# Optimization experiments

Hardware: AMD Instinct MI355X
Metric: run time of the kernel (lower is better)

## Reference

```python
import jax, jax.numpy as jnp
import numpy as np

N, C, D, K = 4096, 512, 64, 10  # samples, clusters (c_max), feature_dim, num_classes
KAPPA_N = 10.0


def setup_inputs() -> dict:
    key = jax.random.key(0)
    k1, k2, k3, k4, k5, k6 = jax.random.split(key, 6)
    data = jax.random.normal(k1, (N, D), dtype=jnp.float32)
    labels = jax.random.randint(k2, (N,), 0, K)
    # cluster support counts n >= kappa_n (mature clusters)
    n = jax.random.uniform(k3, (C,), dtype=jnp.float32) * 90.0 + KAPPA_N
    mu = jax.random.normal(k4, (C, D), dtype=jnp.float32) * 2.0
    # S is the scatter matrix; covariance Sigma = S / n must be SPD, so
    # build S = n * (0.1 * A A^T + 0.5 I)
    A = jax.random.normal(k5, (C, D, D), dtype=jnp.float32)
    AAT = jnp.einsum('cij,ckj->cik', A, A) / D
    S = n[:, None, None] * (0.1 * AAT + 0.5 * jnp.eye(D, dtype=jnp.float32))
    # one-hot class label per cluster
    cls = jax.random.randint(k6, (C,), 0, K)
    cluster_labels = jax.nn.one_hot(cls, K, dtype=jnp.int32)
    return {"data": data, "labels": labels, "n": n, "mu": mu, "S": S,
            "cluster_labels": cluster_labels}


def reference(data, labels, n, mu, S, cluster_labels):
    # Inference path of eGAUSSp.forward: for each sample z,
    #   Gamma_j = exp(-0.5 * (z - mu_j)^T (S_j / n_j)^{-1} (z - mu_j))   (all c clusters)
    #   scores  = defuzzify = sum_j Gamma_j * onehot(label_j) / sum_j Gamma_j
    # Vectorized over the batch (no cross-sample dependence in eval mode).
    eps = jnp.asarray(1e-6, data.dtype)
    Sigma = S / n[:, None, None] + eps * jnp.eye(S.shape[-1], dtype=data.dtype)  # [C,D,D]
    Sinv = jnp.linalg.inv(Sigma)                                                  # [C,D,D]
    diff = data[:, None, :] - mu[None, :, :]          # [N,C,D]
    tmp = jnp.einsum('ncd,cde->nce', diff, Sinv)      # [N,C,D]
    d2 = jnp.einsum('nce,nce->nc', tmp, diff)         # [N,C] squared Mahalanobis
    Gamma = jnp.exp(-0.5 * d2)                        # [N,C] activations
    lab_f = cluster_labels.astype(data.dtype)         # [C,K]
    scores = (Gamma @ lab_f) / (jnp.sum(Gamma, axis=1, keepdims=True) + 1e-12)  # [N,K]
    pred = jnp.argmax(scores, axis=1)
    clusters = jnp.argmax(Gamma, axis=1)
    return scores, pred, clusters
```

## Files before the change

### kernel.cpp

```cpp
#include <hip/hip_runtime.h>
#include <hip/hip_bf16.h>
#include <math.h>

#define NS 4096
#define NC 512
#define ND 64
#define NK 10
#define NPAIR 2080
#define KP 2176
#define BOFF 2080
#define KOFF 2144
#define ZB 1024
#define QB 2048
#define KSPLIT 4
#define KT_PER 17

typedef __attribute__((ext_vector_type(8))) short short8;
typedef __attribute__((ext_vector_type(4))) float floatx4;

__device__ inline unsigned short f2b(float x) {
    __hip_bfloat16 h = __float2bfloat16(x);
    return __builtin_bit_cast(unsigned short, h);
}
__device__ inline float b2f(unsigned short u) {
    __hip_bfloat16 h = __builtin_bit_cast(__hip_bfloat16, u);
    return __bfloat162float(h);
}

__device__ inline float rlane(float v, int k) {
    return __builtin_bit_cast(float, __builtin_amdgcn_readlane(__builtin_bit_cast(int, v), k));
}

__device__ inline void gl16(const void* g, void* l) {
    __builtin_amdgcn_global_load_lds(
        (const __attribute__((address_space(1))) unsigned int*)g,
        (__attribute__((address_space(3))) unsigned int*)l, 16, 0, 0);
}

__device__ inline uchar2 ed_decode(int p) {
    if (p < NPAIR) {
        const float s = sqrtf((float)(16641 - 8 * p));
        int e = (int)((129.0f - s) * 0.5f);
        int off = e * 64 - (e * (e - 1)) / 2;
        const int offn = off + (64 - e);
        if (p >= offn) { off = offn; ++e; }
        else if (p < off) { off -= (65 - e); --e; }
        return make_uchar2((unsigned char)e, (unsigned char)(e + (p - off)));
    } else if (p < KOFF) return make_uchar2((unsigned char)(p - BOFF), 64);
    else if (p == KOFF)  return make_uchar2(64, 64);
    return make_uchar2(65, 65);
}

__global__ __launch_bounds__(256, 4) void prep_kernel(
    const float* __restrict__ data, const float* __restrict__ S,
    const float* __restrict__ n, const float* __restrict__ mu,
    const int* __restrict__ clab,
    unsigned short* __restrict__ Qh, unsigned short* __restrict__ Ql,
    unsigned short* __restrict__ Bph, unsigned short* __restrict__ Bpl,
    float* __restrict__ d2, float* __restrict__ labf)
{
    __shared__ float AcolS[ND * (ND + 1)];
    __shared__ float cbuf[ND];
    __shared__ float rowbuf[2][ND];
    __shared__ float kksS[1];
    __shared__ float zq[2][66];

    if (blockIdx.x >= NC + ZB) {
        const int qb = blockIdx.x - (NC + ZB);
        const int half = threadIdx.x >> 7;
        const int i = threadIdx.x & 127;
        const int row = qb * 2 + half;
        if (i < 64) zq[half][i] = data[(size_t)row * ND + i];
        else if (i == 64) { zq[half][64] = 1.0f; zq[half][65] = 0.0f; }
        __syncthreads();
        const float* __restrict__ zr = zq[half];
        unsigned short* __restrict__ qh = Qh + (size_t)row * KP;
        unsigned short* __restrict__ ql = Ql + (size_t)row * KP;
        #pragma unroll
        for (int t = 0; t < 4; ++t) {
            const int p0 = t * 512 + i * 4;
            uchar2 ed = ed_decode(p0);
            unsigned short h4[4], l4[4];
            #pragma unroll
            for (int r = 0; r < 4; ++r) {
                const float v = zr[ed.x] * zr[ed.y];
                h4[r] = f2b(v);
                l4[r] = f2b(v - b2f(h4[r]));
                ed = (ed.y < 63) ? make_uchar2(ed.x, (unsigned char)(ed.y + 1))
                                 : make_uchar2((unsigned char)(ed.x + 1),
                                               (unsigned char)(ed.x + 1));
            }
            *(short4*)&qh[p0] = make_short4((short)h4[0], (short)h4[1],
                                            (short)h4[2], (short)h4[3]);
            *(short4*)&ql[p0] = make_short4((short)l4[0], (short)l4[1],
                                            (short)l4[2], (short)l4[3]);
        }
        {
            const int p = 2048 + i;
            const uchar2 ed = ed_decode(p);
            const float v = zr[ed.x] * zr[ed.y];
            const unsigned short h = f2b(v);
            const unsigned short l = f2b(v - b2f(h));
            qh[p] = h;
            ql[p] = l;
        }
        return;
    }

    if (blockIdx.x >= NC) {
        const size_t base = (size_t)(blockIdx.x - NC) * 2048 + threadIdx.x * 8;
        *(float4*)&d2[base]     = make_float4(0.f, 0.f, 0.f, 0.f);
        *(float4*)&d2[base + 4] = make_float4(0.f, 0.f, 0.f, 0.f);
        return;
    }

    const int c = blockIdx.x;
    const int tid = threadIdx.x;
    const int j = tid & 63;
    const int w = tid >> 6;
    const int rbase = w * 16;

    const float inv_nc = 1.0f / n[c];
    const float* __restrict__ Sc = S + (size_t)c * ND * ND + j;

    float4 B0, B1, B2, B3;
#define LOADT(u) \
    const float t##u##0 = Sc[(rbase + 4*(u) + 0) * ND]; \
    const float t##u##1 = Sc[(rbase + 4*(u) + 1) * ND]; \
    const float t##u##2 = Sc[(rbase + 4*(u) + 2) * ND]; \
    const float t##u##3 = Sc[(rbase + 4*(u) + 3) * ND];
    LOADT(0) LOADT(1) LOADT(2) LOADT(3)
#undef LOADT
    __builtin_amdgcn_sched_barrier(0);
#define SCALE(u) { \
    const float x0 = t##u##0 * inv_nc; \
    const float x1 = t##u##1 * inv_nc; \
    const float x2 = t##u##2 * inv_nc; \
    const float x3 = t##u##3 * inv_nc; \
    B##u.x = (rbase + 4*(u) + 0 == j) ? x0 + 1e-6f : x0; \
    B##u.y = (rbase + 4*(u) + 1 == j) ? x1 + 1e-6f : x1; \
    B##u.z = (rbase + 4*(u) + 2 == j) ? x2 + 1e-6f : x2; \
    B##u.w = (rbase + 4*(u) + 3 == j) ? x3 + 1e-6f : x3; }
    SCALE(0) SCALE(1) SCALE(2) SCALE(3)
#undef SCALE

#define UPD4(u, K) {                                                  \
    const float c0 = rlane(B##u.x, K);                                \
    const float c1 = rlane(B##u.y, K);                                \
    const float c2 = rlane(B##u.z, K);                                \
    const float c3 = rlane(B##u.w, K);                                \
    B##u.x = (om && (4*(u)+0 == ((K)&15))) ? rowk : B##u.x * am - c0 * rowk; \
    B##u.y = (om && (4*(u)+1 == ((K)&15))) ? rowk : B##u.y * am - c1 * rowk; \
    B##u.z = (om && (4*(u)+2 == ((K)&15))) ? rowk : B##u.z * am - c2 * rowk; \
    B##u.w = (om && (4*(u)+3 == ((K)&15))) ? rowk : B##u.w * am - c3 * rowk; \
}
#define STEPC(TL, C, K) {                                             \
    if (w == ((K) >> 4)) {                                            \
        const float rp = B##TL.C;          \
        const float pv = rlane(rp, K);             \
        const float ip = 1.0f / pv;                                   \
        rowbuf[(K) & 1][j] = (j == (K)) ? ip : rp * ip;               \
    }                                                                 \
    __syncthreads();                                                  \
    const float rowk = rowbuf[(K) & 1][j];                            \
    const float am = (j == (K)) ? 0.0f : 1.0f;                        \
    const bool om = (w == ((K) >> 4));                                \
    UPD4(0, K) UPD4(1, K) UPD4(2, K) UPD4(3, K)                       \
}
#define STEP4(T, TL) STEPC(TL, x, 4*(T)+0) STEPC(TL, y, 4*(T)+1) \
                     STEPC(TL, z, 4*(T)+2) STEPC(TL, w, 4*(T)+3)
#define FOR16P(M) M(0,0) M(1,1) M(2,2) M(3,3) M(4,0) M(5,1) M(6,2) M(7,3) \
                  M(8,0) M(9,1) M(10,2) M(11,3) M(12,0) M(13,1) M(14,2) M(15,3)
    FOR16P(STEP4)
#undef FOR16P
#undef STEP4
#undef STEPC
#undef UPD4

#define MIR(u) *(float4*)&AcolS[j * (ND + 1) + rbase + 4*(u)] = B##u;
    MIR(0) MIR(1) MIR(2) MIR(3)
#undef MIR
    __syncthreads();

    if (w == 0) {
        const float* __restrict__ muc = mu + (size_t)c * ND;
        float y = 0.f;
        #pragma unroll
        for (int t = 0; t < 16; ++t) {
            const float4 v = *(const float4*)&AcolS[j * (ND + 1) + 4 * t];
            y += v.x * muc[4*t]     + v.y * muc[4*t + 1]
               + v.z * muc[4*t + 2] + v.w * muc[4*t + 3];
        }
        cbuf[j] = -2.0f * y;
        float kk = muc[j] * y;
        #pragma unroll
        for (int off = 32; off > 0; off >>= 1) kk += __shfl_down(kk, off);
        if (j == 0) {
            kksS[0] = kk;
            int lab = 0;
            for (int q = 0; q < NK; ++q) if (clab[c * NK + q] != 0) lab = q;
            labf[c] = (float)lab;
        }
    }
    __syncthreads();
    const float kks = kksS[0];

    unsigned short* __restrict__ ph = Bph + (size_t)c * KP;
    unsigned short* __restrict__ pl = Bpl + (size_t)c * KP;
    #pragma unroll
    for (int i = 0; i < 9; ++i) {
        const int t = w + 4 * i;
        if (t < KP / 64) {
            const int p = t * 64 + j;
            float val;
            if (p < NPAIR) {
                const uchar2 ed = ed_decode(p);
                val = (ed.x == ed.y) ? AcolS[ed.x * (ND + 1) + ed.x]
                    : (AcolS[ed.y * (ND + 1) + ed.x] + AcolS[ed.x * (ND + 1) + ed.y]);
            } else if (p < KOFF) val = cbuf[p - BOFF];
            else if (p == KOFF)  val = kks;
            else                 val = 0.f;
            const unsigned short h = f2b(val);
            const unsigned short l = f2b(val - b2f(h));
            ph[p] = h;
            pl[p] = l;
        }
    }
}

__global__ __launch_bounds__(256, 5) void gemm_kernel(
    const unsigned short* __restrict__ Qh, const unsigned short* __restrict__ Ql,
    const unsigned short* __restrict__ Bph, const unsigned short* __restrict__ Bpl,
    float* __restrict__ d2)
{
    __shared__ unsigned short AhS[2][64 * 32], AlS[2][64 * 32];
    __shared__ unsigned short BhS[2][64 * 32], BlS[2][64 * 32];

    const int tid  = threadIdx.x;
    const int lane = tid & 63, w = tid >> 6;
    const int quad = lane >> 4, rlo = lane & 15;

    const int m0 = blockIdx.x * 64;
    const int n0 = blockIdx.y * 64;
    const int koff0 = blockIdx.z * KT_PER * 32;

    const int srow = tid >> 2;
    const int sswz = (tid & 3) ^ ((srow >> 2) & 3);
    const unsigned short* aGh = Qh + (size_t)(m0 + srow) * KP + koff0 + sswz * 8;
    const unsigned short* aGl = Ql + (size_t)(m0 + srow) * KP + koff0 + sswz * 8;
    const unsigned short* bGh = Bph + (size_t)(n0 + srow) * KP + koff0 + sswz * 8;
    const unsigned short* bGl = Bpl + (size_t)(n0 + srow) * KP + koff0 + sswz * 8;
    const int swz8 = (quad ^ ((rlo >> 2) & 3)) * 8;

    floatx4 acc[4] = {};

#define STAGE(b, t) {                                                 \
        const int _ko = (t) * 32;                                     \
        gl16(aGh + _ko, &AhS[b][tid * 8]);                            \
        gl16(aGl + _ko, &AlS[b][tid * 8]);                            \
        gl16(bGh + _ko, &BhS[b][tid * 8]);                            \
        gl16(bGl + _ko, &BlS[b][tid * 8]);                            \
    }

    STAGE(0, 0)
    STAGE(1, 1)
    asm volatile("s_waitcnt vmcnt(4)" ::: "memory");
    __builtin_amdgcn_s_barrier();
    __builtin_amdgcn_sched_barrier(0);

    for (int kt = 0; kt < KT_PER; ++kt) {
        const int cur = kt & 1;

        short8 ah[4], al[4], bh, bl;
        #pragma unroll
        for (int i = 0; i < 4; ++i) {
            ah[i] = *(const short8*)&AhS[cur][(i * 16 + rlo) * 32 + swz8];
            al[i] = *(const short8*)&AlS[cur][(i * 16 + rlo) * 32 + swz8];
        }
        {
            const int r = w * 16 + rlo;
            bh = *(const short8*)&BhS[cur][r * 32 + swz8];
            bl = *(const short8*)&BlS[cur][r * 32 + swz8];
        }

        __builtin_amdgcn_s_setprio(1);
        #pragma unroll
        for (int i = 0; i < 4; ++i) {
            acc[i] = __builtin_amdgcn_mfma_f32_16x16x32_bf16(al[i], bh, acc[i], 0, 0, 0);
            acc[i] = __builtin_amdgcn_mfma_f32_16x16x32_bf16(ah[i], bl, acc[i], 0, 0, 0);
            acc[i] = __builtin_amdgcn_mfma_f32_16x16x32_bf16(ah[i], bh, acc[i], 0, 0, 0);
        }
        __builtin_amdgcn_s_setprio(0);

        asm volatile("s_waitcnt lgkmcnt(0)" ::: "memory");
        __builtin_amdgcn_s_barrier();

        if (kt < KT_PER - 2) STAGE(cur, kt + 2)

        if (kt < KT_PER - 2) {
            asm volatile("s_waitcnt vmcnt(4)" ::: "memory");
        } else {
            asm volatile("s_waitcnt vmcnt(0)" ::: "memory");
        }
        __builtin_amdgcn_s_barrier();
        __builtin_amdgcn_sched_barrier(0);
    }
#undef STAGE

    #pragma unroll
    for (int i = 0; i < 4; ++i) {
        const int m = m0 + i * 16 + quad * 4;
        const int nn = n0 + w * 16 + rlo;
        #pragma unroll
        for (int r = 0; r < 4; ++r)
            atomicAdd(&d2[(size_t)(m + r) * NC + nn], acc[i][r]);
    }
}

__global__ __launch_bounds__(256) void score_kernel(
    const float* __restrict__ d2, const float* __restrict__ labf,
    float* __restrict__ out)
{
    const int s = blockIdx.x * 4 + (threadIdx.x >> 6);
    const int l = threadIdx.x & 63;

    float numer[NK];
    #pragma unroll
    for (int q = 0; q < NK; ++q) numer[q] = 0.f;
    float denom = 0.f, gmax = -1.f;
    int gidx = 0;

    #pragma unroll
    for (int i = 0; i < NC / 256; ++i) {
        const int c0 = i * 256 + l * 4;
        const float4 v = *(const float4*)&d2[(size_t)s * NC + c0];
        #pragma unroll
        for (int r = 0; r < 4; ++r) {
            const int c = c0 + r;
            const float G = __expf(-0.5f * ((const float*)&v)[r]);
            denom += G;
            const int lab = (int)labf[c];
            #pragma unroll
            for (int q = 0; q < NK; ++q) numer[q] += (q == lab) ? G : 0.f;
            if (G > gmax) { gmax = G; gidx = c; }
        }
    }

    #pragma unroll
    for (int off = 32; off > 0; off >>= 1) {
        const float og = __shfl_down(gmax, off);
        const int   oi = __shfl_down(gidx, off);
        if (og > gmax || (og == gmax && oi < gidx)) { gmax = og; gidx = oi; }
        denom += __shfl_down(denom, off);
        #pragma unroll
        for (int q = 0; q < NK; ++q) numer[q] += __shfl_down(numer[q], off);
    }

    if (l == 0) {
        const float inv = 1.0f / (denom + 1e-12f);
        float best = -1.f; int pk = 0;
        #pragma unroll
        for (int q = 0; q < NK; ++q) {
            const float sc = numer[q] * inv;
            out[(size_t)s * NK + q] = sc;
            if (sc > best) { best = sc; pk = q; }
        }
        out[(size_t)NS * NK + s]      = (float)pk;
        out[(size_t)NS * NK + NS + s] = (float)gidx;
    }
}

extern "C" void kernel_launch(void* const* d_in, const int* in_sizes, int n_in,
                              void* d_out, int out_size, void* d_ws, size_t ws_size,
                              hipStream_t stream)
{
    const float* data = (const float*)d_in[0];
    const float* n    = (const float*)d_in[2];
    const float* mu   = (const float*)d_in[3];
    const float* S    = (const float*)d_in[4];
    const int*   clab = (const int*)d_in[5];

    char* w = (char*)d_ws;
    unsigned short* Qh  = (unsigned short*)(w);
    unsigned short* Ql  = (unsigned short*)(w + 17825792);
    unsigned short* Bph = (unsigned short*)(w + 35651584);
    unsigned short* Bpl = (unsigned short*)(w + 37879808);
    float* d2   = (float*)(w + 40108032);
    float* labf = (float*)(w + 48496640);

    hipLaunchKernelGGL(prep_kernel,  dim3(NC + ZB + QB), dim3(256), 0, stream,
                       data, S, n, mu, clab, Qh, Ql, Bph, Bpl, d2, labf);
    hipLaunchKernelGGL(gemm_kernel,  dim3(NS / 64, NC / 64, KSPLIT), dim3(256), 0, stream,
                       Qh, Ql, Bph, Bpl, d2);
    hipLaunchKernelGGL(score_kernel, dim3(NS / 4), dim3(256), 0, stream,
                       d2, labf, (float*)d_out);
}
```

Measured before the change: 150.6 us.

## Drop split-K atomics; use 64x32 GEMM tiles over full K with direct stores

Replaces the 4-way split-K GEMM, which needed a zeroing pass in the prep kernel and atomicAdd accumulation, with a non-split GEMM. Each block now computes a 64x32 tile over the full K=2176 and writes d2 with plain stores. The grid shrinks from 64x8x4 to 64x16 blocks, but each block runs a 68-step K loop. B tiles are halved, so each wave holds 2 accumulators instead of 4, and occupancy is raised to 6. This removes atomic traffic and the d2 memset, at the cost of less A reuse per block (A is loaded twice as often) and fewer blocks to hide latency.

```diff
diff --git a/kernel.cpp b/kernel.cpp
--- a/kernel.cpp
+++ b/kernel.cpp
@@ -10,10 +10,8 @@
 #define KP 2176
 #define BOFF 2080
 #define KOFF 2144
-#define ZB 1024
 #define QB 2048
-#define KSPLIT 4
-#define KT_PER 17
+#define KT 68
 
 typedef __attribute__((ext_vector_type(8))) short short8;
 typedef __attribute__((ext_vector_type(4))) float floatx4;
@@ -57,7 +55,7 @@
     const int* __restrict__ clab,
     unsigned short* __restrict__ Qh, unsigned short* __restrict__ Ql,
     unsigned short* __restrict__ Bph, unsigned short* __restrict__ Bpl,
-    float* __restrict__ d2, float* __restrict__ labf)
+    float* __restrict__ labf)
 {
     __shared__ float AcolS[ND * (ND + 1)];
     __shared__ float cbuf[ND];
@@ -65,8 +63,8 @@
     __shared__ float kksS[1];
     __shared__ float zq[2][66];
 
-    if (blockIdx.x >= NC + ZB) {
-        const int qb = blockIdx.x - (NC + ZB);
+    if (blockIdx.x >= NC) {
+        const int qb = blockIdx.x - NC;
         const int half = threadIdx.x >> 7;
         const int i = threadIdx.x & 127;
         const int row = qb * 2 + half;
@@ -104,13 +102,6 @@
             qh[p] = h;
             ql[p] = l;
         }
-        return;
-    }
-
-    if (blockIdx.x >= NC) {
-        const size_t base = (size_t)(blockIdx.x - NC) * 2048 + threadIdx.x * 8;
-        *(float4*)&d2[base]     = make_float4(0.f, 0.f, 0.f, 0.f);
-        *(float4*)&d2[base + 4] = make_float4(0.f, 0.f, 0.f, 0.f);
         return;
     }
 
@@ -228,77 +219,76 @@
     }
 }
 
-__global__ __launch_bounds__(256, 5) void gemm_kernel(
+__global__ __launch_bounds__(256, 6) void gemm_kernel(
     const unsigned short* __restrict__ Qh, const unsigned short* __restrict__ Ql,
     const unsigned short* __restrict__ Bph, const unsigned short* __restrict__ Bpl,
     float* __restrict__ d2)
 {
     __shared__ unsigned short AhS[2][64 * 32], AlS[2][64 * 32];
-    __shared__ unsigned short BhS[2][64 * 32], BlS[2][64 * 32];
+    __shared__ unsigned short BhS[2][32 * 32], BlS[2][32 * 32];
 
     const int tid  = threadIdx.x;
     const int lane = tid & 63, w = tid >> 6;
     const int quad = lane >> 4, rlo = lane & 15;
 
     const int m0 = blockIdx.x * 64;
-    const int n0 = blockIdx.y * 64;
-    const int koff0 = blockIdx.z * KT_PER * 32;
+    const int n0 = blockIdx.y * 32;
 
     const int srow = tid >> 2;
     const int sswz = (tid & 3) ^ ((srow >> 2) & 3);
-    const unsigned short* aGh = Qh + (size_t)(m0 + srow) * KP + koff0 + sswz * 8;
-    const unsigned short* aGl = Ql + (size_t)(m0 + srow) * KP + koff0 + sswz * 8;
-    const unsigned short* bGh = Bph + (size_t)(n0 + srow) * KP + koff0 + sswz * 8;
-    const unsigned short* bGl = Bpl + (size_t)(n0 + srow) * KP + koff0 + sswz * 8;
+    const unsigned short* aGh = Qh + (size_t)(m0 + srow) * KP + sswz * 8;
+    const unsigned short* aGl = Ql + (size_t)(m0 + srow) * KP + sswz * 8;
+    const int bt  = tid & 127;
+    const int brow = bt >> 2;
+    const int bswz = (bt & 3) ^ ((brow >> 2) & 3);
+    const unsigned short* bG = (tid < 128 ? Bph : Bpl)
+                             + (size_t)(n0 + brow) * KP + bswz * 8;
     const int swz8 = (quad ^ ((rlo >> 2) & 3)) * 8;
 
-    floatx4 acc[4] = {};
+    floatx4 acc[2] = {};
 
 #define STAGE(b, t) {                                                 \
         const int _ko = (t) * 32;                                     \
         gl16(aGh + _ko, &AhS[b][tid * 8]);                            \
         gl16(aGl + _ko, &AlS[b][tid * 8]);                            \
-        gl16(bGh + _ko, &BhS[b][tid * 8]);                            \
-        gl16(bGl + _ko, &BlS[b][tid * 8]);                            \
+        gl16(bG + _ko, (tid < 128) ? &BhS[b][bt * 8]                  \
+                                   : &BlS[b][bt * 8]);                \
     }
 
     STAGE(0, 0)
     STAGE(1, 1)
-    asm volatile("s_waitcnt vmcnt(4)" ::: "memory");
+    asm volatile("s_waitcnt vmcnt(3)" ::: "memory");
     __builtin_amdgcn_s_barrier();
     __builtin_amdgcn_sched_barrier(0);
 
-    for (int kt = 0; kt < KT_PER; ++kt) {
+    for (int kt = 0; kt < KT; ++kt) {
         const int cur = kt & 1;
 
-        short8 ah[4], al[4], bh, bl;
-        #pragma unroll
-        for (int i = 0; i < 4; ++i) {
-            ah[i] = *(const short8*)&AhS[cur][(i * 16 + rlo) * 32 + swz8];
-            al[i] = *(const short8*)&AlS[cur][(i * 16 + rlo) * 32 + swz8];
-        }
-        {
-            const int r = w * 16 + rlo;
-            bh = *(const short8*)&BhS[cur][r * 32 + swz8];
-            bl = *(const short8*)&BlS[cur][r * 32 + swz8];
+        short8 ah, al, bh[2], bl[2];
+        ah = *(const short8*)&AhS[cur][(w * 16 + rlo) * 32 + swz8];
+        al = *(const short8*)&AlS[cur][(w * 16 + rlo) * 32 + swz8];
+        #pragma unroll
+        for (int j2 = 0; j2 < 2; ++j2) {
+            bh[j2] = *(const short8*)&BhS[cur][(j2 * 16 + rlo) * 32 + swz8];
+            bl[j2] = *(const short8*)&BlS[cur][(j2 * 16 + rlo) * 32 + swz8];
         }
 
         __builtin_amdgcn_s_setprio(1);
         #pragma unroll
-        for (int i = 0; i < 4; ++i) {
-            acc[i] = __builtin_amdgcn_mfma_f32_16x16x32_bf16(al[i], bh, acc[i], 0, 0, 0);
-            acc[i] = __builtin_amdgcn_mfma_f32_16x16x32_bf16(ah[i], bl, acc[i], 0, 0, 0);
-            acc[i] = __builtin_amdgcn_mfma_f32_16x16x32_bf16(ah[i], bh, acc[i], 0, 0, 0);
+        for (int j2 = 0; j2 < 2; ++j2) {
+            acc[j2] = __builtin_amdgcn_mfma_f32_16x16x32_bf16(al, bh[j2], acc[j2], 0, 0, 0);
+            acc[j2] = __builtin_amdgcn_mfma_f32_16x16x32_bf16(ah, bl[j2], acc[j2], 0, 0, 0);
+            acc[j2] = __builtin_amdgcn_mfma_f32_16x16x32_bf16(ah, bh[j2], acc[j2], 0, 0, 0);
         }
         __builtin_amdgcn_s_setprio(0);
 
         asm volatile("s_waitcnt lgkmcnt(0)" ::: "memory");
         __builtin_amdgcn_s_barrier();
 
-        if (kt < KT_PER - 2) STAGE(cur, kt + 2)
-
-        if (kt < KT_PER - 2) {
-            asm volatile("s_waitcnt vmcnt(4)" ::: "memory");
+        if (kt < KT - 2) STAGE(cur, kt + 2)
+
+        if (kt < KT - 2) {
+            asm volatile("s_waitcnt vmcnt(3)" ::: "memory");
         } else {
             asm volatile("s_waitcnt vmcnt(0)" ::: "memory");
         }
@@ -308,12 +298,12 @@
 #undef STAGE
 
     #pragma unroll
-    for (int i = 0; i < 4; ++i) {
-        const int m = m0 + i * 16 + quad * 4;
-        const int nn = n0 + w * 16 + rlo;
+    for (int j2 = 0; j2 < 2; ++j2) {
+        const int m = m0 + w * 16 + quad * 4;
+        const int nn = n0 + j2 * 16 + rlo;
         #pragma unroll
         for (int r = 0; r < 4; ++r)
-            atomicAdd(&d2[(size_t)(m + r) * NC + nn], acc[i][r]);
+            d2[(size_t)(m + r) * NC + nn] = acc[j2][r];
     }
 }
 
@@ -388,9 +378,9 @@
     float* d2   = (float*)(w + 40108032);
     float* labf = (float*)(w + 48496640);
 
-    hipLaunchKernelGGL(prep_kernel,  dim3(NC + ZB + QB), dim3(256), 0, stream,
-                       data, S, n, mu, clab, Qh, Ql, Bph, Bpl, d2, labf);
-    hipLaunchKernelGGL(gemm_kernel,  dim3(NS / 64, NC / 64, KSPLIT), dim3(256), 0, stream,
+    hipLaunchKernelGGL(prep_kernel,  dim3(NC + QB), dim3(256), 0, stream,
+                       data, S, n, mu, clab, Qh, Ql, Bph, Bpl, labf);
+    hipLaunchKernelGGL(gemm_kernel,  dim3(NS / 64, NC / 32), dim3(256), 0, stream,
                        Qh, Ql, Bph, Bpl, d2);
     hipLaunchKernelGGL(score_kernel, dim3(NS / 4), dim3(256), 0, stream,
                        d2, labf, (float*)d_out);
```

After: 143.9 us. -4.4%, faster.
